# Kernel tuning notes

Hardware: AMD Instinct MI355X
Metric: run time of the kernel (lower is better)

The kernel has to match this reference:

```python
import jax, jax.numpy as jnp
import numpy as np
from jax import lax

DIM = 768
HEADS = 12
EXPERTS = 4
CAPS = [0.4, 0.3, 0.2, 0.1]  # capacity fraction per expert e=0..E-1 (e=E-1 is the full-dim expert)
EPS = 1e-5


def _layernorm(x, g, b):
    mu = jnp.mean(x, axis=-1, keepdims=True)
    var = jnp.mean(jnp.square(x - mu), axis=-1, keepdims=True)
    return (x - mu) * lax.rsqrt(var + EPS) * g + b


def _route(x, router_w, router_b):
    # Expert-preferred capacity router: experts (largest dim first) greedily take
    # their top-capacity tokens by router probability among still-unassigned tokens.
    B, N, _ = x.shape
    probs = jax.nn.softmax(x @ router_w + router_b, axis=-1)  # [B,N,E]
    ks = [int(c * N) for c in CAPS]
    ks[-1] += N - sum(ks)  # remainder to the largest expert
    assigned = jnp.zeros((B, N), dtype=jnp.int32)
    avail = jnp.ones((B, N), dtype=bool)
    brow = jnp.arange(B)[:, None]
    for e in reversed(range(EXPERTS)):
        pe = jnp.where(avail, probs[:, :, e], -jnp.inf)
        _, idx = lax.top_k(pe, ks[e])  # [B, k_e]
        sel = jnp.zeros((B, N), dtype=bool).at[brow, idx].set(True)
        assigned = jnp.where(sel, e, assigned)
        avail = avail & ~sel
    router_probs = jnp.take_along_axis(probs, assigned[..., None], axis=-1)[..., 0]  # [B,N]
    return assigned, router_probs


def _feat_mask(token_mask, dtype):
    # expert e uses the first DIM / 2^(E-1-e) features (nested slicing)
    dims = jnp.array([DIM >> (EXPERTS - 1 - e) for e in range(EXPERTS)], dtype=jnp.int32)
    d_tok = dims[token_mask]  # [B,N]
    return (jnp.arange(DIM)[None, None, :] < d_tok[..., None]).astype(dtype)  # [B,N,D]


def _nested_attention(h, mask, wqkv, bqkv, wo, bo):
    # masking input + output of a full projection == using the top-left nested submatrix
    B, N, D = h.shape
    hd = D // HEADS
    qkv = ((h * mask) @ wqkv + bqkv) * jnp.tile(mask, (1, 1, 3))  # [B,N,3D]
    q, k, v = jnp.split(qkv, 3, axis=-1)
    q = q.reshape(B, N, HEADS, hd).transpose(0, 2, 1, 3)  # [B,H,N,hd]
    k = k.reshape(B, N, HEADS, hd).transpose(0, 2, 1, 3)
    v = v.reshape(B, N, HEADS, hd).transpose(0, 2, 1, 3)
    scores = jnp.einsum('bhqd,bhkd->bhqk', q, k) * (hd ** -0.5)
    attn = jax.nn.softmax(scores, axis=-1)
    out = jnp.einsum('bhqk,bhkd->bhqd', attn, v)  # [B,H,N,hd]
    out = out.transpose(0, 2, 1, 3).reshape(B, N, D) * mask
    return ((out @ wo) + bo) * mask


def setup_inputs() -> dict:
    key = jax.random.key(0)
    ks = jax.random.split(key, 8)
    B, N, D = 4, 1024, DIM
    s = 0.02
    return {
        'x': jax.random.normal(ks[0], (B, N, D), jnp.float32),
        'ln1_g': jnp.ones((D,), jnp.float32),
        'ln1_b': jnp.zeros((D,), jnp.float32),
        'router_w': jax.random.normal(ks[1], (D, EXPERTS), jnp.float32) * s,
        'router_b': jnp.zeros((EXPERTS,), jnp.float32),
        'wqkv': jax.random.normal(ks[2], (D, 3 * D), jnp.float32) * s,
        'bqkv': jnp.zeros((3 * D,), jnp.float32),
        'wo': jax.random.normal(ks[3], (D, D), jnp.float32) * s,
        'bo': jnp.zeros((D,), jnp.float32),
        'ln2_g': jnp.ones((D,), jnp.float32),
        'ln2_b': jnp.zeros((D,), jnp.float32),
        'w1': jax.random.normal(ks[4], (D, 4 * D), jnp.float32) * s,
        'b1': jnp.zeros((4 * D,), jnp.float32),
        'w2': jax.random.normal(ks[5], (4 * D, D), jnp.float32) * s,
        'b2': jnp.zeros((D,), jnp.float32),
    }


def reference(x, ln1_g, ln1_b, router_w, router_b, wqkv, bqkv, wo, bo,
              ln2_g, ln2_b, w1, b1, w2, b2):
    token_mask, router_probs = _route(x, router_w, router_b)
    mask = _feat_mask(token_mask, x.dtype)  # [B,N,D]
    z = x + _nested_attention(_layernorm(x, ln1_g, ln1_b), mask, wqkv, bqkv, wo, bo)
    h2 = _layernorm(z, ln2_g, ln2_b)
    z_prime = jax.nn.gelu(h2 @ w1 + b1, approximate=False) @ w2 + b2
    # probability-weighted token combine
    return z + router_probs[..., None] * z_prime
```

## Files before the change

### kernel.cpp

```cpp
#include <hip/hip_runtime.h>
#include <math.h>

#define DIM 768
#define NTOK 1024
#define BATCH 4
#define HEADS 12
#define TOKENS (BATCH * NTOK)

typedef __bf16 bf16;
typedef __attribute__((ext_vector_type(8))) __bf16 bf16x8;
typedef __attribute__((ext_vector_type(4))) float floatx4;

__global__ void router_kernel(const float* __restrict__ x,
                              const float* __restrict__ rw,
                              const float* __restrict__ rb,
                              float* __restrict__ probs) {
    int t = blockIdx.x;
    int tid = threadIdx.x;
    const float* xr = x + (size_t)t * DIM;
    double acc[4] = {0, 0, 0, 0};
    for (int k = tid; k < DIM; k += 256) {
        double xv = (double)xr[k];
        acc[0] += xv * (double)rw[k * 4 + 0];
        acc[1] += xv * (double)rw[k * 4 + 1];
        acc[2] += xv * (double)rw[k * 4 + 2];
        acc[3] += xv * (double)rw[k * 4 + 3];
    }
    __shared__ double red[256];
    __shared__ double logits[4];
    for (int e = 0; e < 4; ++e) {
        red[tid] = acc[e];
        __syncthreads();
        for (int s = 128; s > 0; s >>= 1) {
            if (tid < s) red[tid] += red[tid + s];
            __syncthreads();
        }
        if (tid == 0) logits[e] = red[0] + (double)rb[e];
        __syncthreads();
    }
    if (tid == 0) {
        double m = logits[0];
        for (int e = 1; e < 4; ++e) m = fmax(m, logits[e]);
        double s = 0.0, p[4];
        for (int e = 0; e < 4; ++e) { p[e] = exp(logits[e] - m); s += p[e]; }
        for (int e = 0; e < 4; ++e) probs[(size_t)t * 4 + e] = (float)(p[e] / s);
    }
}

template <int E, int KCAP, bool FIRST, bool LAST>
__global__ __launch_bounds__(256) void route_pass(const float* __restrict__ probs,
                                                  int* __restrict__ avail,
                                                  int* __restrict__ dtok_g,
                                                  float* __restrict__ rprobs_g) {
    int b = blockIdx.y;
    int i = blockIdx.x * 256 + threadIdx.x;
    const float* pb = probs + (size_t)b * NTOK * 4;
    __shared__ float sp[1024];
    for (int j = threadIdx.x; j < 1024; j += 256) {
        bool av = FIRST ? true : (avail[b * NTOK + j] != 0);
        sp[j] = av ? pb[j * 4 + E] : -INFINITY;
    }
    __syncthreads();
    bool av_i = FIRST ? true : (avail[b * NTOK + i] != 0);
    float pi = sp[i];
    int cnt = 0;
#pragma unroll 8
    for (int j0 = 0; j0 < 1024; j0 += 4) {
        floatx4 pj = *(const floatx4*)&sp[j0];
        cnt += (pj[0] > pi) || (pj[0] == pi && (j0 + 0) < i);
        cnt += (pj[1] > pi) || (pj[1] == pi && (j0 + 1) < i);
        cnt += (pj[2] > pi) || (pj[2] == pi && (j0 + 2) < i);
        cnt += (pj[3] > pi) || (pj[3] == pi && (j0 + 3) < i);
    }
    bool sel = av_i && (cnt < KCAP);
    if (sel) {
        dtok_g[b * NTOK + i] = DIM >> (3 - E);
        rprobs_g[b * NTOK + i] = pb[i * 4 + E];
    } else if (LAST && av_i) {
        dtok_g[b * NTOK + i] = DIM >> 3;
        rprobs_g[b * NTOK + i] = pb[i * 4 + 0];
    }
    if (!LAST) {
        if (FIRST) avail[b * NTOK + i] = sel ? 0 : 1;
        else if (sel) avail[b * NTOK + i] = 0;
    }
}

__global__ void ln_mask_kernel(const float* __restrict__ x,
                               const float* __restrict__ g,
                               const float* __restrict__ bta,
                               const int* __restrict__ dtok,
                               bf16* __restrict__ out) {
    int t = blockIdx.x;
    int tid = threadIdx.x;
    const float* xr = x + (size_t)t * DIM;
    float s = 0.0f;
    for (int k = tid; k < DIM; k += 256) s += xr[k];
    __shared__ float red[256];
    red[tid] = s;
    __syncthreads();
    for (int st = 128; st > 0; st >>= 1) {
        if (tid < st) red[tid] += red[tid + st];
        __syncthreads();
    }
    float mu = red[0] / DIM;
    __syncthreads();
    float v = 0.0f;
    for (int k = tid; k < DIM; k += 256) { float d = xr[k] - mu; v += d * d; }
    red[tid] = v;
    __syncthreads();
    for (int st = 128; st > 0; st >>= 1) {
        if (tid < st) red[tid] += red[tid + st];
        __syncthreads();
    }
    float rs = rsqrtf(red[0] / DIM + 1e-5f);
    int d = dtok ? dtok[t] : DIM;
    for (int k = tid; k < DIM; k += 256) {
        float val = (xr[k] - mu) * rs * g[k] + bta[k];
        out[(size_t)t * DIM + k] = (bf16)((k < d) ? val : 0.0f);
    }
}

__global__ __launch_bounds__(256) void transpose_bf16_kernel(const float* __restrict__ W,
                                                             bf16* __restrict__ Wt,
                                                             int K, int N) {
    __shared__ float t[32][33];
    int bx = blockIdx.x * 32;
    int by = blockIdx.y * 32;
    int tx = threadIdx.x, ty = threadIdx.y;
#pragma unroll
    for (int i = 0; i < 4; ++i)
        t[ty + i * 8][tx] = W[(size_t)(by + ty + i * 8) * N + bx + tx];
    __syncthreads();
#pragma unroll
    for (int i = 0; i < 4; ++i)
        Wt[(size_t)(bx + ty + i * 8) * K + by + tx] = (bf16)t[tx][ty + i * 8];
}

#define LDT 40
template <int MODE>
__global__ __launch_bounds__(256) void gemm_mfma(const bf16* __restrict__ A,
                                                 const bf16* __restrict__ Bt,
                                                 const float* __restrict__ bias,
                                                 void* __restrict__ Cout,
                                                 int M, int NN, int K, int Kc,
                                                 const int* __restrict__ dtok,
                                                 const float* __restrict__ aux,
                                                 const float* __restrict__ rp) {
    __shared__ bf16 As[2][128 * LDT];
    __shared__ bf16 Bs[2][128 * LDT];
    int n0 = blockIdx.x * 128;
    int m0 = blockIdx.y * 128;
    int kbase = blockIdx.z * Kc;
    int tid = threadIdx.x;
    int wv = tid >> 6;
    int lane = tid & 63;
    int l16 = lane & 15, q4 = lane >> 4;
    int wm = (wv >> 1) * 64, wn = (wv & 1) * 64;
    const bf16* Ap = A + (size_t)m0 * K + kbase;
    const bf16* Bp = Bt + (size_t)n0 * K + kbase;
    floatx4 pa[2], pb[2];
#pragma unroll
    for (int u = 0; u < 2; ++u) {
        int s = tid + u * 256, row = s >> 2, part = s & 3;
        pa[u] = *(const floatx4*)&Ap[(size_t)row * K + part * 8];
        pb[u] = *(const floatx4*)&Bp[(size_t)row * K + part * 8];
    }
#pragma unroll
    for (int u = 0; u < 2; ++u) {
        int s = tid + u * 256, row = s >> 2, part = s & 3;
        *(floatx4*)&As[0][row * LDT + part * 8] = pa[u];
        *(floatx4*)&Bs[0][row * LDT + part * 8] = pb[u];
    }
    __syncthreads();
    floatx4 acc[4][4] = {};
    int kIters = Kc / 32;
    int cur = 0;
    for (int it = 0; it < kIters; ++it) {
        bool notlast = (it + 1 < kIters);
        if (notlast) {
            int ko = (it + 1) * 32;
#pragma unroll
            for (int u = 0; u < 2; ++u) {
                int s = tid + u * 256, row = s >> 2, part = s & 3;
                pa[u] = *(const floatx4*)&Ap[(size_t)row * K + ko + part * 8];
                pb[u] = *(const floatx4*)&Bp[(size_t)row * K + ko + part * 8];
            }
        }
        bf16x8 af[4], bfr[4];
#pragma unroll
        for (int t = 0; t < 4; ++t) {
            af[t] = *(const bf16x8*)&As[cur][(wm + t * 16 + l16) * LDT + q4 * 8];
            bfr[t] = *(const bf16x8*)&Bs[cur][(wn + t * 16 + l16) * LDT + q4 * 8];
        }
#pragma unroll
        for (int i = 0; i < 4; ++i)
#pragma unroll
            for (int j = 0; j < 4; ++j)
                acc[i][j] = __builtin_amdgcn_mfma_f32_16x16x32_bf16(af[i], bfr[j], acc[i][j], 0, 0, 0);
        if (notlast) {
#pragma unroll
            for (int u = 0; u < 2; ++u) {
                int s = tid + u * 256, row = s >> 2, part = s & 3;
                *(floatx4*)&As[cur ^ 1][row * LDT + part * 8] = pa[u];
                *(floatx4*)&Bs[cur ^ 1][row * LDT + part * 8] = pb[u];
            }
            __syncthreads();
            cur ^= 1;
        }
    }
#pragma unroll
    for (int i = 0; i < 4; ++i) {
#pragma unroll
        for (int j = 0; j < 4; ++j) {
            int col = n0 + wn + j * 16 + l16;
#pragma unroll
            for (int r = 0; r < 4; ++r) {
                int row = m0 + wm + i * 16 + q4 * 4 + r;
                if (MODE == 4) {
                    ((float*)Cout)[(size_t)blockIdx.z * M * NN + (size_t)row * NN + col] =
                        acc[i][j][r];
                    continue;
                }
                float c = acc[i][j][r] + bias[col];
                if (MODE == 0) {
                    int jm = col % 768;
                    c = (jm < dtok[row]) ? c : 0.0f;
                    ((bf16*)Cout)[(size_t)row * NN + col] = (bf16)c;
                } else if (MODE == 1) {
                    c = (col < dtok[row]) ? c : 0.0f;
                    c += aux[(size_t)row * NN + col];
                    ((float*)Cout)[(size_t)row * NN + col] = c;
                } else if (MODE == 2) {
                    c = 0.5f * c * (1.0f + erff(c * 0.70710678118654752f));
                    ((bf16*)Cout)[(size_t)row * NN + col] = (bf16)c;
                } else if (MODE == 3) {
                    c = aux[(size_t)row * NN + col] + rp[row] * c;
                    ((float*)Cout)[(size_t)row * NN + col] = c;
                }
            }
        }
    }
}

__global__ __launch_bounds__(256) void ffn2_reduce(const float* __restrict__ part,
                                                   const float* __restrict__ z,
                                                   const float* __restrict__ bias,
                                                   const float* __restrict__ rp,
                                                   float* __restrict__ out) {
    size_t idx = ((size_t)blockIdx.x * 256 + threadIdx.x) * 4;
    int row = (int)(idx / DIM);
    int col = (int)(idx % DIM);
    floatx4 p0 = *(const floatx4*)&part[idx];
    floatx4 p1 = *(const floatx4*)&part[(size_t)TOKENS * DIM + idx];
    floatx4 zz = *(const floatx4*)&z[idx];
    floatx4 bb = *(const floatx4*)&bias[col];
    float r = rp[row];
    floatx4 o = zz + (p0 + p1 + bb) * r;
    *(floatx4*)&out[idx] = o;
}

#define LDH 72
__global__ __launch_bounds__(256) void attn_mfma(const bf16* __restrict__ qkv,
                                                 const int* __restrict__ dtok,
                                                 bf16* __restrict__ attno) {
    int qt = blockIdx.x;
    int h = blockIdx.y;
    int b = blockIdx.z;
    int tid = threadIdx.x;
    int wv = tid >> 6;
    int lane = tid & 63;
    int l16 = lane & 15, q4 = lane >> 4;
    __shared__ bf16 Qs[64 * LDH];
    __shared__ bf16 Ks[64 * LDH];
    __shared__ bf16 Vt[64 * LDH];
    __shared__ bf16 Ps[4][16 * LDH];
    size_t base = (size_t)b * NTOK * 2304;
    for (int s = tid; s < 512; s += 256) {
        int row = s >> 3, part = s & 7;
        *(floatx4*)&Qs[row * LDH + part * 8] =
            *(const floatx4*)&qkv[base + (size_t)(qt * 64 + row) * 2304 + h * 64 + part * 8];
    }
    floatx4 o[4] = {};
    float m_r[4] = {-INFINITY, -INFINITY, -INFINITY, -INFINITY};
    float l_r[4] = {0.0f, 0.0f, 0.0f, 0.0f};
    for (int kt = 0; kt < 16; ++kt) {
        __syncthreads();
        for (int s = tid; s < 512; s += 256) {
            int row = s >> 3, part = s & 7;
            *(floatx4*)&Ks[row * LDH + part * 8] =
                *(const floatx4*)&qkv[base + (size_t)(kt * 64 + row) * 2304 + 768 + h * 64 + part * 8];
            floatx4 vv =
                *(const floatx4*)&qkv[base + (size_t)(kt * 64 + row) * 2304 + 1536 + h * 64 + part * 8];
            const bf16* vp = (const bf16*)&vv;
#pragma unroll
            for (int j = 0; j < 8; ++j) Vt[(part * 8 + j) * LDH + row] = vp[j];
        }
        __syncthreads();
        floatx4 sc[4] = {};
#pragma unroll
        for (int ch = 0; ch < 2; ++ch) {
            bf16x8 aq = *(const bf16x8*)&Qs[(wv * 16 + l16) * LDH + ch * 32 + q4 * 8];
#pragma unroll
            for (int nt = 0; nt < 4; ++nt) {
                bf16x8 bk = *(const bf16x8*)&Ks[(nt * 16 + l16) * LDH + ch * 32 + q4 * 8];
                sc[nt] = __builtin_amdgcn_mfma_f32_16x16x32_bf16(aq, bk, sc[nt], 0, 0, 0);
            }
        }
        float alpha[4], psum[4];
#pragma unroll
        for (int r = 0; r < 4; ++r) {
            float v0 = fmaxf(fmaxf(sc[0][r], sc[1][r]), fmaxf(sc[2][r], sc[3][r])) * 0.125f;
#pragma unroll
            for (int msk = 1; msk < 16; msk <<= 1) v0 = fmaxf(v0, __shfl_xor(v0, msk));
            float mn = fmaxf(m_r[r], v0);
            alpha[r] = __expf(m_r[r] - mn);
            m_r[r] = mn;
            psum[r] = 0.0f;
        }
#pragma unroll
        for (int nt = 0; nt < 4; ++nt)
#pragma unroll
            for (int r = 0; r < 4; ++r) {
                float p = __expf(sc[nt][r] * 0.125f - m_r[r]);
                psum[r] += p;
                Ps[wv][(q4 * 4 + r) * LDH + nt * 16 + l16] = (bf16)p;
            }
#pragma unroll
        for (int r = 0; r < 4; ++r) {
            float s = psum[r];
#pragma unroll
            for (int msk = 1; msk < 16; msk <<= 1) s += __shfl_xor(s, msk);
            l_r[r] = l_r[r] * alpha[r] + s;
        }
#pragma unroll
        for (int dt = 0; dt < 4; ++dt)
#pragma unroll
            for (int r = 0; r < 4; ++r) o[dt][r] *= alpha[r];
        __syncthreads();
#pragma unroll
        for (int ch = 0; ch < 2; ++ch) {
            bf16x8 ap = *(const bf16x8*)&Ps[wv][l16 * LDH + ch * 32 + q4 * 8];
#pragma unroll
            for (int dt = 0; dt < 4; ++dt) {
                bf16x8 bv = *(const bf16x8*)&Vt[(dt * 16 + l16) * LDH + ch * 32 + q4 * 8];
                o[dt] = __builtin_amdgcn_mfma_f32_16x16x32_bf16(ap, bv, o[dt], 0, 0, 0);
            }
        }
    }
#pragma unroll
    for (int r = 0; r < 4; ++r) {
        int tokrow = qt * 64 + wv * 16 + q4 * 4 + r;
        int dt_tok = dtok[b * NTOK + tokrow];
        float inv = 1.0f / l_r[r];
#pragma unroll
        for (int dt = 0; dt < 4; ++dt) {
            int col = h * 64 + dt * 16 + l16;
            float val = (col < dt_tok) ? o[dt][r] * inv : 0.0f;
            attno[((size_t)b * NTOK + tokrow) * DIM + col] = (bf16)val;
        }
    }
}

extern "C" void kernel_launch(void* const* d_in, const int* in_sizes, int n_in,
                              void* d_out, int out_size, void* d_ws, size_t ws_size,
                              hipStream_t stream) {
    const float* x = (const float*)d_in[0];
    const float* ln1g = (const float*)d_in[1];
    const float* ln1b = (const float*)d_in[2];
    const float* rw = (const float*)d_in[3];
    const float* rb = (const float*)d_in[4];
    const float* wqkv = (const float*)d_in[5];
    const float* bqkv = (const float*)d_in[6];
    const float* wo = (const float*)d_in[7];
    const float* bo = (const float*)d_in[8];
    const float* ln2g = (const float*)d_in[9];
    const float* ln2b = (const float*)d_in[10];
    const float* w1 = (const float*)d_in[11];
    const float* b1 = (const float*)d_in[12];
    const float* w2 = (const float*)d_in[13];
    const float* b2 = (const float*)d_in[14];
    float* out = (float*)d_out;

    char* ws = (char*)d_ws;
    size_t off = 0;
    auto alloc = [&](size_t bytes) {
        void* p = ws + off;
        off = (off + bytes + 255) & ~(size_t)255;
        return p;
    };
    bf16* h1m = (bf16*)alloc(sizeof(bf16) * TOKENS * DIM);
    float* probs = (float*)alloc(sizeof(float) * TOKENS * 4);
    float* rprobs = (float*)alloc(sizeof(float) * TOKENS);
    int* dtok = (int*)alloc(sizeof(int) * TOKENS);
    int* avail = (int*)alloc(sizeof(int) * TOKENS);
    bf16* qkvb = (bf16*)alloc(sizeof(bf16) * TOKENS * 3 * DIM);
    bf16* attno = (bf16*)alloc(sizeof(bf16) * TOKENS * DIM);
    float* z = (float*)alloc(sizeof(float) * TOKENS * DIM);
    bf16* h2 = (bf16*)alloc(sizeof(bf16) * TOKENS * DIM);
    bf16* ffn1 = (bf16*)alloc(sizeof(bf16) * TOKENS * 4 * DIM);
    bf16* wqkvT = (bf16*)alloc(sizeof(bf16) * DIM * 3 * DIM);
    bf16* woT = (bf16*)alloc(sizeof(bf16) * DIM * DIM);
    bf16* w1T = (bf16*)alloc(sizeof(bf16) * DIM * 4 * DIM);
    bf16* w2T = (bf16*)alloc(sizeof(bf16) * 4 * DIM * DIM);
    float* part = (float*)alloc(sizeof(float) * 2 * TOKENS * DIM);

    dim3 tb(32, 8);
    transpose_bf16_kernel<<<dim3(2304 / 32, 768 / 32), tb, 0, stream>>>(wqkv, wqkvT, 768, 2304);
    transpose_bf16_kernel<<<dim3(768 / 32, 768 / 32), tb, 0, stream>>>(wo, woT, 768, 768);
    transpose_bf16_kernel<<<dim3(3072 / 32, 768 / 32), tb, 0, stream>>>(w1, w1T, 768, 3072);
    transpose_bf16_kernel<<<dim3(768 / 32, 3072 / 32), tb, 0, stream>>>(w2, w2T, 3072, 768);

    router_kernel<<<TOKENS, 256, 0, stream>>>(x, rw, rb, probs);
    route_pass<3, 104, true, false><<<dim3(4, BATCH), 256, 0, stream>>>(probs, avail, dtok, rprobs);
    route_pass<2, 204, false, false><<<dim3(4, BATCH), 256, 0, stream>>>(probs, avail, dtok, rprobs);
    route_pass<1, 307, false, true><<<dim3(4, BATCH), 256, 0, stream>>>(probs, avail, dtok, rprobs);
    ln_mask_kernel<<<TOKENS, 256, 0, stream>>>(x, ln1g, ln1b, dtok, h1m);
    gemm_mfma<0><<<dim3(2304 / 128, 4096 / 128), 256, 0, stream>>>(
        h1m, wqkvT, bqkv, qkvb, TOKENS, 2304, 768, 768, dtok, nullptr, nullptr);
    attn_mfma<<<dim3(16, 12, 4), 256, 0, stream>>>(qkvb, dtok, attno);
    gemm_mfma<1><<<dim3(768 / 128, 4096 / 128), 256, 0, stream>>>(
        attno, woT, bo, z, TOKENS, 768, 768, 768, dtok, x, nullptr);
    ln_mask_kernel<<<TOKENS, 256, 0, stream>>>(z, ln2g, ln2b, nullptr, h2);
    gemm_mfma<2><<<dim3(3072 / 128, 4096 / 128), 256, 0, stream>>>(
        h2, w1T, b1, ffn1, TOKENS, 3072, 768, 768, nullptr, nullptr, nullptr);
    gemm_mfma<4><<<dim3(768 / 128, 4096 / 128, 2), 256, 0, stream>>>(
        ffn1, w2T, nullptr, part, TOKENS, 768, 3072, 1536, nullptr, nullptr, nullptr);
    ffn2_reduce<<<TOKENS * DIM / 1024, 256, 0, stream>>>(part, z, b2, rprobs, out);
}
```

Measured before the change: 444.0 us.

## Use async global-to-LDS loads in GEMM, pre-transpose V, fuse Wo epilogue with LN2

The GEMM drops its register-staged double-buffered LDS pipeline and loads tiles with global_load_lds directly into a single LDS buffer, with a barrier before and after each k-step. V is transposed once into a separate buffer so attention can copy it straight in, and K/V tiles are now prefetched into registers. The Wo projection becomes a split-K GEMM whose reduction, bias, mask, residual add and LayerNorm2 are fused into one new kernel, removing a separate LN pass. The trade-off is that the single-buffered async loads leave global latency exposed in every GEMM, and there is an extra transpose kernel plus extra partial-sum traffic for Wo.

Measured after the change: 435.6 us. No clear change (-1.9%).

```diff
diff --git a/kernel.cpp b/kernel.cpp
--- a/kernel.cpp
+++ b/kernel.cpp
@@ -10,6 +10,11 @@
 typedef __bf16 bf16;
 typedef __attribute__((ext_vector_type(8))) __bf16 bf16x8;
 typedef __attribute__((ext_vector_type(4))) float floatx4;
+
+__device__ __forceinline__ void async_ld16(const bf16* g, bf16* l) {
+    __builtin_amdgcn_global_load_lds((const __attribute__((address_space(1))) unsigned int*)g,
+                                     (__attribute__((address_space(3))) unsigned int*)l, 16, 0, 0);
+}
 
 __global__ void router_kernel(const float* __restrict__ x,
                               const float* __restrict__ rw,
@@ -121,6 +126,56 @@
     }
 }
 
+__global__ __launch_bounds__(256) void wo_ln2_kernel(const float* __restrict__ part,
+                                                     const float* __restrict__ x,
+                                                     const float* __restrict__ bo,
+                                                     const int* __restrict__ dtok,
+                                                     const float* __restrict__ g,
+                                                     const float* __restrict__ bta,
+                                                     float* __restrict__ z,
+                                                     bf16* __restrict__ h2) {
+    int t = blockIdx.x;
+    int tid = threadIdx.x;
+    int d = dtok[t];
+    float vals[3];
+    float s = 0.0f;
+#pragma unroll
+    for (int i = 0; i < 3; ++i) {
+        int k = i * 256 + tid;
+        float c = (k < d) ? (part[(size_t)t * DIM + k] +
+                             part[(size_t)TOKENS * DIM + (size_t)t * DIM + k] + bo[k])
+                          : 0.0f;
+        c += x[(size_t)t * DIM + k];
+        vals[i] = c;
+        s += c;
+    }
+    __shared__ float red[256];
+    red[tid] = s;
+    __syncthreads();
+    for (int st = 128; st > 0; st >>= 1) {
+        if (tid < st) red[tid] += red[tid + st];
+        __syncthreads();
+    }
+    float mu = red[0] / DIM;
+    __syncthreads();
+    float v = 0.0f;
+#pragma unroll
+    for (int i = 0; i < 3; ++i) { float dd = vals[i] - mu; v += dd * dd; }
+    red[tid] = v;
+    __syncthreads();
+    for (int st = 128; st > 0; st >>= 1) {
+        if (tid < st) red[tid] += red[tid + st];
+        __syncthreads();
+    }
+    float rs = rsqrtf(red[0] / DIM + 1e-5f);
+#pragma unroll
+    for (int i = 0; i < 3; ++i) {
+        int k = i * 256 + tid;
+        z[(size_t)t * DIM + k] = vals[i];
+        h2[(size_t)t * DIM + k] = (bf16)((vals[i] - mu) * rs * g[k] + bta[k]);
+    }
+}
+
 __global__ __launch_bounds__(256) void transpose_bf16_kernel(const float* __restrict__ W,
                                                              bf16* __restrict__ Wt,
                                                              int K, int N) {
@@ -137,18 +192,43 @@
         Wt[(size_t)(bx + ty + i * 8) * K + by + tx] = (bf16)t[tx][ty + i * 8];
 }
 
-#define LDT 40
+__global__ __launch_bounds__(256) void vt_trans_kernel(const bf16* __restrict__ qkv,
+                                                       bf16* __restrict__ vtg) {
+    int nt = blockIdx.x;
+    int h = blockIdx.y;
+    int b = blockIdx.z;
+    int tid = threadIdx.x;
+    __shared__ bf16 T[64 * 72];
+    size_t base = (size_t)b * NTOK * 2304;
+#pragma unroll
+    for (int u = 0; u < 2; ++u) {
+        int e = u * 256 + tid;
+        int row = e >> 3, part = e & 7;
+        *(floatx4*)&T[row * 72 + part * 8] =
+            *(const floatx4*)&qkv[base + (size_t)(nt * 64 + row) * 2304 + 1536 + h * 64 + part * 8];
+    }
+    __syncthreads();
+    size_t vbase = ((size_t)(b * HEADS + h)) * 64 * NTOK;
+#pragma unroll
+    for (int u = 0; u < 2; ++u) {
+        int e = u * 256 + tid;
+        int d = e >> 3, ng = e & 7;
+        bf16 tmp[8];
+#pragma unroll
+        for (int j = 0; j < 8; ++j) tmp[j] = T[(ng * 8 + j) * 72 + d];
+        *(floatx4*)&vtg[vbase + (size_t)d * NTOK + nt * 64 + ng * 8] = *(floatx4*)tmp;
+    }
+}
+
 template <int MODE>
 __global__ __launch_bounds__(256) void gemm_mfma(const bf16* __restrict__ A,
                                                  const bf16* __restrict__ Bt,
                                                  const float* __restrict__ bias,
                                                  void* __restrict__ Cout,
                                                  int M, int NN, int K, int Kc,
-                                                 const int* __restrict__ dtok,
-                                                 const float* __restrict__ aux,
-                                                 const float* __restrict__ rp) {
-    __shared__ bf16 As[2][128 * LDT];
-    __shared__ bf16 Bs[2][128 * LDT];
+                                                 const int* __restrict__ dtok) {
+    __shared__ bf16 As[128 * 32];
+    __shared__ bf16 Bs[128 * 32];
     int n0 = blockIdx.x * 128;
     int m0 = blockIdx.y * 128;
     int kbase = blockIdx.z * Kc;
@@ -157,57 +237,36 @@
     int lane = tid & 63;
     int l16 = lane & 15, q4 = lane >> 4;
     int wm = (wv >> 1) * 64, wn = (wv & 1) * 64;
-    const bf16* Ap = A + (size_t)m0 * K + kbase;
-    const bf16* Bp = Bt + (size_t)n0 * K + kbase;
-    floatx4 pa[2], pb[2];
-#pragma unroll
-    for (int u = 0; u < 2; ++u) {
-        int s = tid + u * 256, row = s >> 2, part = s & 3;
-        pa[u] = *(const floatx4*)&Ap[(size_t)row * K + part * 8];
-        pb[u] = *(const floatx4*)&Bp[(size_t)row * K + part * 8];
-    }
-#pragma unroll
-    for (int u = 0; u < 2; ++u) {
-        int s = tid + u * 256, row = s >> 2, part = s & 3;
-        *(floatx4*)&As[0][row * LDT + part * 8] = pa[u];
-        *(floatx4*)&Bs[0][row * LDT + part * 8] = pb[u];
-    }
-    __syncthreads();
+    int srow = lane >> 2, scol = (lane & 3) * 8;
+    const bf16* gA0 = A + (size_t)(m0 + 32 * wv + srow) * K + kbase + scol;
+    const bf16* gB0 = Bt + (size_t)(n0 + 32 * wv + srow) * K + kbase + scol;
+    const bf16* gA1 = gA0 + (size_t)16 * K;
+    const bf16* gB1 = gB0 + (size_t)16 * K;
+    bf16* lA0 = &As[(32 * wv) * 32];
+    bf16* lA1 = &As[(32 * wv + 16) * 32];
+    bf16* lB0 = &Bs[(32 * wv) * 32];
+    bf16* lB1 = &Bs[(32 * wv + 16) * 32];
     floatx4 acc[4][4] = {};
     int kIters = Kc / 32;
-    int cur = 0;
     for (int it = 0; it < kIters; ++it) {
-        bool notlast = (it + 1 < kIters);
-        if (notlast) {
-            int ko = (it + 1) * 32;
-#pragma unroll
-            for (int u = 0; u < 2; ++u) {
-                int s = tid + u * 256, row = s >> 2, part = s & 3;
-                pa[u] = *(const floatx4*)&Ap[(size_t)row * K + ko + part * 8];
-                pb[u] = *(const floatx4*)&Bp[(size_t)row * K + ko + part * 8];
-            }
-        }
+        __syncthreads();
+        async_ld16(gA0, lA0);
+        async_ld16(gA1, lA1);
+        async_ld16(gB0, lB0);
+        async_ld16(gB1, lB1);
+        gA0 += 32; gA1 += 32; gB0 += 32; gB1 += 32;
+        __syncthreads();
         bf16x8 af[4], bfr[4];
 #pragma unroll
         for (int t = 0; t < 4; ++t) {
-            af[t] = *(const bf16x8*)&As[cur][(wm + t * 16 + l16) * LDT + q4 * 8];
-            bfr[t] = *(const bf16x8*)&Bs[cur][(wn + t * 16 + l16) * LDT + q4 * 8];
+            af[t] = *(const bf16x8*)&As[(wm + t * 16 + l16) * 32 + q4 * 8];
+            bfr[t] = *(const bf16x8*)&Bs[(wn + t * 16 + l16) * 32 + q4 * 8];
         }
 #pragma unroll
         for (int i = 0; i < 4; ++i)
 #pragma unroll
             for (int j = 0; j < 4; ++j)
                 acc[i][j] = __builtin_amdgcn_mfma_f32_16x16x32_bf16(af[i], bfr[j], acc[i][j], 0, 0, 0);
-        if (notlast) {
-#pragma unroll
-            for (int u = 0; u < 2; ++u) {
-                int s = tid + u * 256, row = s >> 2, part = s & 3;
-                *(floatx4*)&As[cur ^ 1][row * LDT + part * 8] = pa[u];
-                *(floatx4*)&Bs[cur ^ 1][row * LDT + part * 8] = pb[u];
-            }
-            __syncthreads();
-            cur ^= 1;
-        }
     }
 #pragma unroll
     for (int i = 0; i < 4; ++i) {
@@ -220,23 +279,15 @@
                 if (MODE == 4) {
                     ((float*)Cout)[(size_t)blockIdx.z * M * NN + (size_t)row * NN + col] =
                         acc[i][j][r];
-                    continue;
-                }
-                float c = acc[i][j][r] + bias[col];
-                if (MODE == 0) {
+                } else if (MODE == 0) {
+                    float c = acc[i][j][r] + bias[col];
                     int jm = col % 768;
                     c = (jm < dtok[row]) ? c : 0.0f;
                     ((bf16*)Cout)[(size_t)row * NN + col] = (bf16)c;
-                } else if (MODE == 1) {
-                    c = (col < dtok[row]) ? c : 0.0f;
-                    c += aux[(size_t)row * NN + col];
-                    ((float*)Cout)[(size_t)row * NN + col] = c;
                 } else if (MODE == 2) {
+                    float c = acc[i][j][r] + bias[col];
                     c = 0.5f * c * (1.0f + erff(c * 0.70710678118654752f));
                     ((bf16*)Cout)[(size_t)row * NN + col] = (bf16)c;
-                } else if (MODE == 3) {
-                    c = aux[(size_t)row * NN + col] + rp[row] * c;
-                    ((float*)Cout)[(size_t)row * NN + col] = c;
                 }
             }
         }
@@ -262,6 +313,7 @@
 
 #define LDH 72
 __global__ __launch_bounds__(256) void attn_mfma(const bf16* __restrict__ qkv,
+                                                 const bf16* __restrict__ vtg,
                                                  const int* __restrict__ dtok,
                                                  bf16* __restrict__ attno) {
     int qt = blockIdx.x;
@@ -276,27 +328,42 @@
     __shared__ bf16 Vt[64 * LDH];
     __shared__ bf16 Ps[4][16 * LDH];
     size_t base = (size_t)b * NTOK * 2304;
-    for (int s = tid; s < 512; s += 256) {
-        int row = s >> 3, part = s & 7;
+    size_t vbase = ((size_t)(b * HEADS + h)) * 64 * NTOK;
+    int erow = tid >> 3, epart = tid & 7;
+#pragma unroll
+    for (int u = 0; u < 2; ++u) {
+        int row = (u * 256 + tid) >> 3, part = (u * 256 + tid) & 7;
         *(floatx4*)&Qs[row * LDH + part * 8] =
             *(const floatx4*)&qkv[base + (size_t)(qt * 64 + row) * 2304 + h * 64 + part * 8];
     }
     floatx4 o[4] = {};
     float m_r[4] = {-INFINITY, -INFINITY, -INFINITY, -INFINITY};
     float l_r[4] = {0.0f, 0.0f, 0.0f, 0.0f};
+    floatx4 kreg[2], vreg[2];
+#pragma unroll
+    for (int u = 0; u < 2; ++u) {
+        int row = (u * 256 + tid) >> 3, part = (u * 256 + tid) & 7;
+        kreg[u] = *(const floatx4*)&qkv[base + (size_t)row * 2304 + 768 + h * 64 + part * 8];
+        vreg[u] = *(const floatx4*)&vtg[vbase + (size_t)row * NTOK + part * 8];
+    }
     for (int kt = 0; kt < 16; ++kt) {
         __syncthreads();
-        for (int s = tid; s < 512; s += 256) {
-            int row = s >> 3, part = s & 7;
-            *(floatx4*)&Ks[row * LDH + part * 8] =
-                *(const floatx4*)&qkv[base + (size_t)(kt * 64 + row) * 2304 + 768 + h * 64 + part * 8];
-            floatx4 vv =
-                *(const floatx4*)&qkv[base + (size_t)(kt * 64 + row) * 2304 + 1536 + h * 64 + part * 8];
-            const bf16* vp = (const bf16*)&vv;
-#pragma unroll
-            for (int j = 0; j < 8; ++j) Vt[(part * 8 + j) * LDH + row] = vp[j];
-        }
-        __syncthreads();
+#pragma unroll
+        for (int u = 0; u < 2; ++u) {
+            int row = (u * 256 + tid) >> 3, part = (u * 256 + tid) & 7;
+            *(floatx4*)&Ks[row * LDH + part * 8] = kreg[u];
+            *(floatx4*)&Vt[row * LDH + part * 8] = vreg[u];
+        }
+        __syncthreads();
+        if (kt < 15) {
+#pragma unroll
+            for (int u = 0; u < 2; ++u) {
+                int row = (u * 256 + tid) >> 3, part = (u * 256 + tid) & 7;
+                kreg[u] = *(const floatx4*)&qkv[base + (size_t)((kt + 1) * 64 + row) * 2304 + 768 +
+                                                h * 64 + part * 8];
+                vreg[u] = *(const floatx4*)&vtg[vbase + (size_t)row * NTOK + (kt + 1) * 64 + part * 8];
+            }
+        }
         floatx4 sc[4] = {};
 #pragma unroll
         for (int ch = 0; ch < 2; ++ch) {
@@ -337,7 +404,6 @@
         for (int dt = 0; dt < 4; ++dt)
 #pragma unroll
             for (int r = 0; r < 4; ++r) o[dt][r] *= alpha[r];
-        __syncthreads();
 #pragma unroll
         for (int ch = 0; ch < 2; ++ch) {
             bf16x8 ap = *(const bf16x8*)&Ps[wv][l16 * LDH + ch * 32 + q4 * 8];
@@ -360,6 +426,7 @@
             attno[((size_t)b * NTOK + tokrow) * DIM + col] = (bf16)val;
         }
     }
+    (void)erow; (void)epart;
 }
 
 extern "C" void kernel_launch(void* const* d_in, const int* in_sizes, int n_in,
@@ -395,6 +462,7 @@
     int* dtok = (int*)alloc(sizeof(int) * TOKENS);
     int* avail = (int*)alloc(sizeof(int) * TOKENS);
     bf16* qkvb = (bf16*)alloc(sizeof(bf16) * TOKENS * 3 * DIM);
+    bf16* vtg = (bf16*)alloc(sizeof(bf16) * BATCH * HEADS * 64 * NTOK);
     bf16* attno = (bf16*)alloc(sizeof(bf16) * TOKENS * DIM);
     float* z = (float*)alloc(sizeof(float) * TOKENS * DIM);
     bf16* h2 = (bf16*)alloc(sizeof(bf16) * TOKENS * DIM);
@@ -417,14 +485,15 @@
     route_pass<1, 307, false, true><<<dim3(4, BATCH), 256, 0, stream>>>(probs, avail, dtok, rprobs);
     ln_mask_kernel<<<TOKENS, 256, 0, stream>>>(x, ln1g, ln1b, dtok, h1m);
     gemm_mfma<0><<<dim3(2304 / 128, 4096 / 128), 256, 0, stream>>>(
-        h1m, wqkvT, bqkv, qkvb, TOKENS, 2304, 768, 768, dtok, nullptr, nullptr);
-    attn_mfma<<<dim3(16, 12, 4), 256, 0, stream>>>(qkvb, dtok, attno);
-    gemm_mfma<1><<<dim3(768 / 128, 4096 / 128), 256, 0, stream>>>(
-        attno, woT, bo, z, TOKENS, 768, 768, 768, dtok, x, nullptr);
-    ln_mask_kernel<<<TOKENS, 256, 0, stream>>>(z, ln2g, ln2b, nullptr, h2);
+        h1m, wqkvT, bqkv, qkvb, TOKENS, 2304, 768, 768, dtok);
+    vt_trans_kernel<<<dim3(16, HEADS, BATCH), 256, 0, stream>>>(qkvb, vtg);
+    attn_mfma<<<dim3(16, HEADS, BATCH), 256, 0, stream>>>(qkvb, vtg, dtok, attno);
+    gemm_mfma<4><<<dim3(768 / 128, 4096 / 128, 2), 256, 0, stream>>>(
+        attno, woT, nullptr, part, TOKENS, 768, 768, 384, nullptr);
+    wo_ln2_kernel<<<TOKENS, 256, 0, stream>>>(part, x, bo, dtok, ln2g, ln2b, z, h2);
     gemm_mfma<2><<<dim3(3072 / 128, 4096 / 128), 256, 0, stream>>>(
-        h2, w1T, b1, ffn1, TOKENS, 3072, 768, 768, nullptr, nullptr, nullptr);
+        h2, w1T, b1, ffn1, TOKENS, 3072, 768, 768, nullptr);
     gemm_mfma<4><<<dim3(768 / 128, 4096 / 128, 2), 256, 0, stream>>>(
-        ffn1, w2T, nullptr, part, TOKENS, 768, 3072, 1536, nullptr, nullptr, nullptr);
+        ffn1, w2T, nullptr, part, TOKENS, 768, 3072, 1536, nullptr);
     ffn2_reduce<<<TOKENS * DIM / 1024, 256, 0, stream>>>(part, z, b2, rprobs, out);
 }
```
